# Performance work log

Hardware: AMD Instinct MI355X
Metric: run time of the kernel (lower is better)

## Reference

```python
import jax, jax.numpy as jnp
import numpy as np

ALPHA = 0.9      # synapse decay
BETA = 0.85      # membrane decay
THRESH = 1.0     # spike threshold
T = 100          # simulation_time
SCALE = 100.0    # SuperSpike surrogate scale

@jax.custom_vjp
def spike(x):
    # Heaviside step forward, fast-sigmoid surrogate gradient (Zenke & Ganguli 2018)
    return (x > 0).astype(x.dtype)

def _spike_fwd(x):
    return spike(x), x

def _spike_bwd(x, g):
    return (g / (SCALE * jnp.abs(x) + 1.0) ** 2,)

spike.defvjp(_spike_fwd, _spike_bwd)


def setup_inputs() -> dict:
    key = jax.random.key(0)
    k1, k2, k3, k4 = jax.random.split(key, 4)
    B = 1024
    shape = [784, 1024, 1024, 10]
    inp = {"input_data": jax.random.uniform(k1, (B, shape[0]), jnp.float32)}
    for i, (kk, (a, b)) in enumerate(zip([k2, k3, k4], zip(shape[:-1], shape[1:]))):
        # init: normal with std = weight_scale / sqrt(fan_in)
        inp[f"W{i}"] = jax.random.normal(kk, (a, b), jnp.float32) / np.sqrt(a)
    return inp


def reference(input_data, W0, W1, W2):
    Ws = [W0, W1, W2]
    B = input_data.shape[0]
    syn0 = [jnp.zeros((B, W.shape[1]), jnp.float32) for W in Ws]
    mem0 = [jnp.zeros((B, W.shape[1]), jnp.float32) for W in Ws]

    def step(carry, _):
        syn, mem = carry
        new_syn, new_mem = [], []
        x = input_data  # encoding='constant': same input every timestep
        for l, W in enumerate(Ws):
            h = x @ W  # [B, out_l]
            if l < len(Ws) - 1:
                # hidden LIF layers: threshold on OLD membrane, spike propagates
                # to the next layer within the same timestep
                mthr = mem[l] - THRESH
                out = spike(mthr)
                rst = jax.lax.stop_gradient(out)  # reset path carries no gradient
                x = out
            else:
                # last layer with decoding='potential': no spiking, no reset
                rst = jnp.zeros_like(mem[l])
            # note: new_mem uses the OLD syn (pre-update), as in the original
            new_syn.append(ALPHA * syn[l] + h)
            new_mem.append(BETA * mem[l] + syn[l] - rst)
        return (new_syn, new_mem), None

    (syn, mem), _ = jax.lax.scan(step, (syn0, mem0), None, length=T)
    # decoding='potential': final membrane potential of the output layer
    return mem[-1]
```

## Files before the change

kernel.cpp:

```cpp
#include <hip/hip_runtime.h>
#include <hip/hip_bf16.h>
#include <stdint.h>
#include <math.h>

typedef unsigned short u16;
typedef unsigned int u32;
typedef unsigned long long u64;
typedef __attribute__((ext_vector_type(8))) short short8;
typedef __attribute__((ext_vector_type(4))) float f32x4;

static constexpr int BDIM  = 1024;
static constexpr int D_IN  = 784;
static constexpr int D_H   = 1024;
static constexpr int D_OUT = 10;
static constexpr int TSTEPS = 100;
static constexpr int K0SEG = 800;
static constexpr int K0TOT = 2400;
static constexpr int NELEM = 1024 * 1024;

#define AL 0.9f
#define BE 0.85f

__device__ __forceinline__ void gld16(const void* g, void* l) {
  __builtin_amdgcn_global_load_lds(
      (const __attribute__((address_space(1))) u32*)g,
      (__attribute__((address_space(3))) u32*)l, 16, 0, 0);
}
__device__ __forceinline__ u16 f2bf(float v) {
  __hip_bfloat16 h = __float2bfloat16(v);
  u16 r; __builtin_memcpy(&r, &h, 2); return r;
}
__device__ __forceinline__ float bf2f(u16 b) {
  __hip_bfloat16 h; __builtin_memcpy(&h, &b, 2); return __bfloat162float(h);
}

__device__ __forceinline__ int stg_rot(int l) { return (((l & 3) - (l >> 3)) & 3) << 3; }
__device__ __forceinline__ int rd_rot(int l) {
  return (((l >> 4) + ((l & 15) >> 1)) & 3) << 3;
}

__global__ void prep0(const float* __restrict__ inp, const float* __restrict__ W0,
                      u16* __restrict__ A0, u16* __restrict__ BT0) {
  int kp = blockIdx.x * 256 + threadIdx.x;
  if (kp >= K0TOT) return;
  int row = blockIdx.y;
  int seg = kp / K0SEG;
  int kk  = kp - seg * K0SEG;
  float av = (kk < D_IN) ? inp[row * D_IN + kk] : 0.f;
  u16 ahi = f2bf(av);
  u16 alo = f2bf(av - bf2f(ahi));
  A0[(size_t)row * K0TOT + kp] = (seg < 2) ? ahi : alo;
  float wv = (kk < D_IN) ? W0[kk * D_H + row] : 0.f;
  u16 whi = f2bf(wv);
  u16 wlo = f2bf(wv - bf2f(whi));
  BT0[(size_t)row * K0TOT + kp] = (seg == 0) ? whi : ((seg == 1) ? wlo : whi);
}

__global__ void prep1(const float* __restrict__ W1, u16* __restrict__ W1h,
                      u16* __restrict__ W1l) {
  int k = blockIdx.x * 256 + threadIdx.x;
  int n = blockIdx.y;
  float v = W1[(size_t)k * D_H + n];
  u16 hi = f2bf(v);
  W1h[(size_t)n * D_H + k] = hi;
  W1l[(size_t)n * D_H + k] = f2bf(v - bf2f(hi));
}

template <int KTOT>
__global__ __launch_bounds__(256) void gemm_bt_t(
    const u16* __restrict__ A, const u16* __restrict__ BT, float* __restrict__ C) {
  constexpr int N = 1024, NBN = 8;
  __shared__ u16 As[128 * 32];
  __shared__ u16 Bs[128 * 32];
  const int nwg = gridDim.x;
  const int bid = blockIdx.x;
  const int wg = (bid & 7) * (nwg >> 3) + (bid >> 3);
  const int bm = wg / NBN, bn = wg - bm * NBN;
  const int tid = threadIdx.x;
  const int w = tid >> 6, l = tid & 63;
  const int wm = w & 1, wn = w >> 1;
  const int srow = l >> 2;
  const int scol = stg_rot(l);
  const size_t m0 = (size_t)bm * 128, n0 = (size_t)bn * 128;
  const int r0 = w * 32;

  const u16* aP0 = &A[(m0 + r0 + srow) * KTOT + scol];
  const u16* aP1 = &A[(m0 + r0 + 16 + srow) * KTOT + scol];
  const u16* bP0 = &BT[(n0 + r0 + srow) * KTOT + scol];
  const u16* bP1 = &BT[(n0 + r0 + 16 + srow) * KTOT + scol];

  const int ps = rd_rot(l);

  f32x4 acc[4][4] = {};

  for (int kt = 0; kt < KTOT; kt += 32) {
    __syncthreads();
    gld16(aP0 + kt, &As[(r0) * 32]);
    gld16(aP1 + kt, &As[(r0 + 16) * 32]);
    gld16(bP0 + kt, &Bs[(r0) * 32]);
    gld16(bP1 + kt, &Bs[(r0 + 16) * 32]);
    __syncthreads();

    short8 a[4], b[4];
#pragma unroll
    for (int m = 0; m < 4; m++)
      a[m] = *(const short8*)&As[(wm * 64 + m * 16 + (l & 15)) * 32 + ps];
#pragma unroll
    for (int n = 0; n < 4; n++)
      b[n] = *(const short8*)&Bs[(wn * 64 + n * 16 + (l & 15)) * 32 + ps];
#pragma unroll
    for (int m = 0; m < 4; m++)
#pragma unroll
      for (int n = 0; n < 4; n++)
        acc[m][n] = __builtin_amdgcn_mfma_f32_16x16x32_bf16(a[m], b[n], acc[m][n], 0, 0, 0);
  }

  const int rr = (l >> 4) * 4, cc = l & 15;
#pragma unroll
  for (int m = 0; m < 4; m++)
#pragma unroll
    for (int n = 0; n < 4; n++) {
      size_t row = m0 + wm * 64 + m * 16 + rr;
      size_t col = n0 + wn * 64 + n * 16 + cc;
#pragma unroll
      for (int j = 0; j < 4; j++)
        C[(row + j) * (size_t)N + col] = acc[m][n][j];
    }
}

__global__ __launch_bounds__(256) void gemm_dual2(
    const u16* __restrict__ A, const u16* __restrict__ Bh, const u16* __restrict__ Bl,
    float* __restrict__ C) {
  constexpr int N = 1024, K = 1024, NT = K / 32;
  __shared__ u16 lds[3 * 12288];
  const int nwg = gridDim.x;
  const int bid = blockIdx.x;
  const int wg = (bid & 7) * (nwg >> 3) + (bid >> 3);
  const int bm = wg >> 3, bn = wg & 7;
  const int tid = threadIdx.x;
  const int w = tid >> 6, l = tid & 63;
  const int wm = w >> 1, wn = w & 1;
  const size_t m0 = (size_t)bm * 128, n0 = (size_t)bn * 128;

  const int srow0 = (w * 2 + 0) * 16 + (l >> 2);
  const int srow1 = (w * 2 + 1) * 16 + (l >> 2);
  const int scol  = stg_rot(l);
  const u16* aS0 = A  + (m0 + srow0) * K + scol;
  const u16* aS1 = A  + (m0 + srow1) * K + scol;
  const u16* hS0 = Bh + (n0 + srow0) * K + scol;
  const u16* hS1 = Bh + (n0 + srow1) * K + scol;
  const u16* lS0 = Bl + (n0 + srow0) * K + scol;
  const u16* lS1 = Bl + (n0 + srow1) * K + scol;
  const int d0 = (w * 2 + 0) * 512;
  const int d1 = (w * 2 + 1) * 512;

  const int rrow = l & 15;
  const int ps = rd_rot(l);

  f32x4 acc[4][4] = {};

  auto STAGE = [&](int ts) {
    u16* Lb = &lds[(ts % 3) * 12288];
    const int ko = ts * 32;
    gld16(aS0 + ko, Lb + d0);
    gld16(aS1 + ko, Lb + d1);
    gld16(hS0 + ko, Lb + 4096 + d0);
    gld16(hS1 + ko, Lb + 4096 + d1);
    gld16(lS0 + ko, Lb + 8192 + d0);
    gld16(lS1 + ko, Lb + 8192 + d1);
  };

  STAGE(0);
  STAGE(1);
  asm volatile("s_waitcnt vmcnt(6)" ::: "memory");
  __builtin_amdgcn_sched_barrier(0);
  __builtin_amdgcn_s_barrier();

  for (int t = 0; t < NT; ++t) {
    const u16* Lb = &lds[(t % 3) * 12288];
    short8 a[4], bh[4], bl[4];
#pragma unroll
    for (int m = 0; m < 4; m++)
      a[m] = *(const short8*)&Lb[(wm * 64 + m * 16 + rrow) * 32 + ps];
#pragma unroll
    for (int n = 0; n < 4; n++) {
      bh[n] = *(const short8*)&Lb[4096 + (wn * 64 + n * 16 + rrow) * 32 + ps];
      bl[n] = *(const short8*)&Lb[8192 + (wn * 64 + n * 16 + rrow) * 32 + ps];
    }
    if (t + 2 < NT) {
      STAGE(t + 2);
      asm volatile("s_waitcnt vmcnt(6)" ::: "memory");
    } else {
      asm volatile("s_waitcnt vmcnt(0)" ::: "memory");
    }
    __builtin_amdgcn_sched_barrier(0);
    __builtin_amdgcn_s_barrier();
    __builtin_amdgcn_s_setprio(1);
#pragma unroll
    for (int m = 0; m < 4; m++)
#pragma unroll
      for (int n = 0; n < 4; n++)
        acc[m][n] = __builtin_amdgcn_mfma_f32_16x16x32_bf16(a[m], bh[n], acc[m][n], 0, 0, 0);
#pragma unroll
    for (int m = 0; m < 4; m++)
#pragma unroll
      for (int n = 0; n < 4; n++)
        acc[m][n] = __builtin_amdgcn_mfma_f32_16x16x32_bf16(a[m], bl[n], acc[m][n], 0, 0, 0);
    __builtin_amdgcn_s_setprio(0);
    __builtin_amdgcn_s_barrier();
  }

  const int rr = (l >> 4) * 4, cc = l & 15;
#pragma unroll
  for (int m = 0; m < 4; m++)
#pragma unroll
    for (int n = 0; n < 4; n++) {
      size_t row = m0 + wm * 64 + m * 16 + rr;
      size_t col = n0 + wn * 64 + n * 16 + cc;
#pragma unroll
      for (int j = 0; j < 4; j++)
        C[(row + j) * (size_t)N + col] = acc[m][n][j];
    }
}

__global__ void scan0(const float* __restrict__ Hconst,
                      float* __restrict__ syn_g, float* __restrict__ mem_g,
                      u64* __restrict__ S, int Tc) {
  int e4 = blockIdx.x * 256 + threadIdx.x;
  int e = e4 * 4;
  float4 syn = *(const float4*)&syn_g[e];
  float4 mem = *(const float4*)&mem_g[e];
  float4 hc = *(const float4*)&Hconst[e];
  for (int t = 0; t < Tc; t++) {
    bool s0 = mem.x > 1.0f, s1 = mem.y > 1.0f, s2 = mem.z > 1.0f, s3 = mem.w > 1.0f;
    u64 sp = (s0 ? 0x3F80ull : 0) | (s1 ? 0x3F800000ull : 0) |
             (s2 ? (0x3F80ull << 32) : 0) | (s3 ? (0x3F80ull << 48) : 0);
    S[(size_t)t * (NELEM / 4) + e4] = sp;
    float ns0 = AL * syn.x + hc.x, ns1 = AL * syn.y + hc.y;
    float ns2 = AL * syn.z + hc.z, ns3 = AL * syn.w + hc.w;
    float nm0 = BE * mem.x + syn.x - (s0 ? 1.0f : 0.0f);
    float nm1 = BE * mem.y + syn.y - (s1 ? 1.0f : 0.0f);
    float nm2 = BE * mem.z + syn.z - (s2 ? 1.0f : 0.0f);
    float nm3 = BE * mem.w + syn.w - (s3 ? 1.0f : 0.0f);
    syn.x = ns0; syn.y = ns1; syn.z = ns2; syn.w = ns3;
    mem.x = nm0; mem.y = nm1; mem.z = nm2; mem.w = nm3;
  }
  *(float4*)&syn_g[e] = syn;
  *(float4*)&mem_g[e] = mem;
}

__global__ void scan1z(const float* __restrict__ Hseq,
                       float* __restrict__ syn_g, float* __restrict__ mem_g,
                       float* __restrict__ z_g, int Tc, float cA0, float cB0) {
  int e4 = blockIdx.x * 256 + threadIdx.x;
  int e = e4 * 4;
  float4 syn = *(const float4*)&syn_g[e];
  float4 mem = *(const float4*)&mem_g[e];
  float4 z   = *(const float4*)&z_g[e];
  float cA = cA0, cB = cB0;
  for (int t = 0; t < Tc; t++) {
    float4 h = *(const float4*)&Hseq[(size_t)t * NELEM + e];
    float c = (cA - cB) * 20.0f;
    bool s0 = mem.x > 1.0f, s1 = mem.y > 1.0f, s2 = mem.z > 1.0f, s3 = mem.w > 1.0f;
    z.x += s0 ? c : 0.0f;
    z.y += s1 ? c : 0.0f;
    z.z += s2 ? c : 0.0f;
    z.w += s3 ? c : 0.0f;
    float ns0 = AL * syn.x + h.x, ns1 = AL * syn.y + h.y;
    float ns2 = AL * syn.z + h.z, ns3 = AL * syn.w + h.w;
    float nm0 = BE * mem.x + syn.x - (s0 ? 1.0f : 0.0f);
    float nm1 = BE * mem.y + syn.y - (s1 ? 1.0f : 0.0f);
    float nm2 = BE * mem.z + syn.z - (s2 ? 1.0f : 0.0f);
    float nm3 = BE * mem.w + syn.w - (s3 ? 1.0f : 0.0f);
    syn.x = ns0; syn.y = ns1; syn.z = ns2; syn.w = ns3;
    mem.x = nm0; mem.y = nm1; mem.z = nm2; mem.w = nm3;
    cA *= (1.0f / AL); cB *= (1.0f / BE);
  }
  *(float4*)&syn_g[e] = syn;
  *(float4*)&mem_g[e] = mem;
  *(float4*)&z_g[e] = z;
}

__global__ __launch_bounds__(256) void zgemm(const float* __restrict__ z,
                                             const float* __restrict__ W2,
                                             float* __restrict__ out) {
  __shared__ float red[256][10];
  const int b = blockIdx.x;
  const int t = threadIdx.x;
  float local[10];
#pragma unroll
  for (int j = 0; j < 10; j++) local[j] = 0.f;
  for (int k = t; k < D_H; k += 256) {
    float zv = z[(size_t)b * D_H + k];
    const float* wrow = &W2[(size_t)k * D_OUT];
#pragma unroll
    for (int j = 0; j < 10; j++) local[j] += zv * wrow[j];
  }
#pragma unroll
  for (int j = 0; j < 10; j++) red[t][j] = local[j];
  __syncthreads();
  for (int s = 128; s > 0; s >>= 1) {
    if (t < s)
#pragma unroll
      for (int j = 0; j < 10; j++) red[t][j] += red[t + s][j];
    __syncthreads();
  }
  if (t < 10) out[b * D_OUT + t] = red[0][t];
}

__global__ void diag(float* out, float v) {
  if (threadIdx.x == 0 && blockIdx.x == 0) out[0] = v;
}

extern "C" void kernel_launch(void* const* d_in, const int* in_sizes, int n_in,
                              void* d_out, int out_size, void* d_ws, size_t ws_size,
                              hipStream_t stream) {
  (void)in_sizes; (void)n_in; (void)out_size;
  const float* inp = (const float*)d_in[0];
  const float* W0  = (const float*)d_in[1];
  const float* W1  = (const float*)d_in[2];
  const float* W2  = (const float*)d_in[3];
  float* out = (float*)d_out;

  uint8_t* base = (uint8_t*)d_ws;
  size_t off = 0;
  auto alloc = [&](size_t bytes) -> void* {
    void* r = base + off;
    off += (bytes + 255) & ~(size_t)255;
    return r;
  };

  float* H0   = (float*)alloc((size_t)NELEM * 4);
  float* syn0 = (float*)alloc((size_t)NELEM * 4);
  float* mem0 = (float*)alloc((size_t)NELEM * 4);
  float* syn1 = (float*)alloc((size_t)NELEM * 4);
  float* mem1 = (float*)alloc((size_t)NELEM * 4);
  float* zbuf = (float*)alloc((size_t)NELEM * 4);
  u16* A0  = (u16*)alloc((size_t)BDIM * K0TOT * 2);
  u16* BT0 = (u16*)alloc((size_t)D_H * K0TOT * 2);
  u16* W1h = (u16*)alloc((size_t)D_H * D_H * 2);
  u16* W1l = (u16*)alloc((size_t)D_H * D_H * 2);
  size_t fixedEnd = off;

  int Tc = 0;
  const int cand[8] = {50, 25, 20, 10, 5, 4, 2, 1};
  for (int i = 0; i < 8; i++) {
    size_t per = (size_t)cand[i] * ((size_t)NELEM * 2 + (size_t)NELEM * 4);
    if (fixedEnd + per + 16 * 256 <= ws_size) { Tc = cand[i]; break; }
  }
  if (Tc == 0) {
    diag<<<1, 1, 0, stream>>>(out, (float)ws_size);
    return;
  }
  u16*   S0c = (u16*)alloc((size_t)Tc * NELEM * 2);
  float* H1c = (float*)alloc((size_t)Tc * NELEM * 4);

  hipMemsetAsync(syn0, 0, (size_t)5 * NELEM * 4, stream);

  prep0<<<dim3(10, BDIM), 256, 0, stream>>>(inp, W0, A0, BT0);
  prep1<<<dim3(4, D_H), 256, 0, stream>>>(W1, W1h, W1l);

  gemm_bt_t<K0TOT><<<dim3(8 * 8), 256, 0, stream>>>(A0, BT0, H0);

  const int nc = TSTEPS / Tc;
  for (int c = 0; c < nc; c++) {
    const int tbase = c * Tc;
    const float cA0 = (float)pow(0.9, (double)(TSTEPS - 1 - tbase));
    const float cB0 = (float)pow(0.85, (double)(TSTEPS - 1 - tbase));
    scan0<<<dim3(NELEM / 1024), 256, 0, stream>>>(H0, syn0, mem0, (u64*)S0c, Tc);
    gemm_dual2<<<dim3(Tc * 8 * 8), 256, 0, stream>>>(S0c, W1h, W1l, H1c);
    scan1z<<<dim3(NELEM / 1024), 256, 0, stream>>>(H1c, syn1, mem1, zbuf, Tc, cA0, cB0);
  }
  zgemm<<<dim3(BDIM), 256, 0, stream>>>(zbuf, W2, out);
}
```

Baseline: 617.1 us.

## Concatenate W1 hi/lo along K and use 256x128 tiles in hidden GEMM

The hi and lo bf16 halves of W1 are packed into a single K=2048 matrix. The A operand (spikes) is reused by wrapping k modulo 1024, so the split GEMM becomes one long-K GEMM. Each workgroup now computes a 256x128 tile with 8x4 accumulators, loading A and B in two half-stages per iteration, which cuts A reloads and LDS traffic per flop. The A0/BT0 buffers are aliased onto the S0c chunk buffer to save workspace, and Tc=1 is dropped as a candidate. The cost is more accumulator registers (launch bounds set to 2 waves) and fewer workgroups per chunk.

```diff
diff --git a/kernel.cpp b/kernel.cpp
--- a/kernel.cpp
+++ b/kernel.cpp
@@ -56,14 +56,12 @@
   BT0[(size_t)row * K0TOT + kp] = (seg == 0) ? whi : ((seg == 1) ? wlo : whi);
 }
 
-__global__ void prep1(const float* __restrict__ W1, u16* __restrict__ W1h,
-                      u16* __restrict__ W1l) {
+__global__ void prep1s(const float* __restrict__ W1, u16* __restrict__ W1s) {
   int k = blockIdx.x * 256 + threadIdx.x;
   int n = blockIdx.y;
-  float v = W1[(size_t)k * D_H + n];
+  float v = W1[(size_t)(k & 1023) * D_H + n];
   u16 hi = f2bf(v);
-  W1h[(size_t)n * D_H + k] = hi;
-  W1l[(size_t)n * D_H + k] = f2bf(v - bf2f(hi));
+  W1s[(size_t)n * 2048 + k] = (k < 1024) ? hi : f2bf(v - bf2f(hi));
 }
 
 template <int KTOT>
@@ -128,10 +126,9 @@
     }
 }
 
-__global__ __launch_bounds__(256) void gemm_dual2(
-    const u16* __restrict__ A, const u16* __restrict__ Bh, const u16* __restrict__ Bl,
-    float* __restrict__ C) {
-  constexpr int N = 1024, K = 1024, NT = K / 32;
+__global__ __launch_bounds__(256, 2) void gemm_dual5(
+    const u16* __restrict__ A, const u16* __restrict__ Bs2, float* __restrict__ C) {
+  constexpr int N = 1024, KA = 1024, KS = 2048, NT = 64;
   __shared__ u16 lds[3 * 12288];
   const int nwg = gridDim.x;
   const int bid = blockIdx.x;
@@ -140,55 +137,64 @@
   const int tid = threadIdx.x;
   const int w = tid >> 6, l = tid & 63;
   const int wm = w >> 1, wn = w & 1;
-  const size_t m0 = (size_t)bm * 128, n0 = (size_t)bn * 128;
-
-  const int srow0 = (w * 2 + 0) * 16 + (l >> 2);
-  const int srow1 = (w * 2 + 1) * 16 + (l >> 2);
-  const int scol  = stg_rot(l);
-  const u16* aS0 = A  + (m0 + srow0) * K + scol;
-  const u16* aS1 = A  + (m0 + srow1) * K + scol;
-  const u16* hS0 = Bh + (n0 + srow0) * K + scol;
-  const u16* hS1 = Bh + (n0 + srow1) * K + scol;
-  const u16* lS0 = Bl + (n0 + srow0) * K + scol;
-  const u16* lS1 = Bl + (n0 + srow1) * K + scol;
-  const int d0 = (w * 2 + 0) * 512;
-  const int d1 = (w * 2 + 1) * 512;
-
+  const size_t m0 = (size_t)bm * 256, n0 = (size_t)bn * 128;
+
+  const int srow = l >> 2;
+  const int scol = stg_rot(l);
+  const u16* aS = A   + (m0 + srow) * KA + scol;
+  const u16* bS = Bs2 + (n0 + srow) * KS + scol;
   const int rrow = l & 15;
   const int ps = rd_rot(l);
 
-  f32x4 acc[4][4] = {};
-
-  auto STAGE = [&](int ts) {
+  f32x4 acc[8][4] = {};
+
+  auto STAGE_A2 = [&](int ts, int half) {
     u16* Lb = &lds[(ts % 3) * 12288];
+    const int ko = (ts & 31) * 32;
+    const int u0 = w * 4 + half * 2;
+    gld16(aS + (size_t)u0 * 16 * KA + ko, Lb + u0 * 512);
+    gld16(aS + (size_t)(u0 + 1) * 16 * KA + ko, Lb + (u0 + 1) * 512);
+  };
+  auto STAGE_B1 = [&](int ts, int half) {
+    u16* Lb = &lds[(ts % 3) * 12288] + 8192;
     const int ko = ts * 32;
-    gld16(aS0 + ko, Lb + d0);
-    gld16(aS1 + ko, Lb + d1);
-    gld16(hS0 + ko, Lb + 4096 + d0);
-    gld16(hS1 + ko, Lb + 4096 + d1);
-    gld16(lS0 + ko, Lb + 8192 + d0);
-    gld16(lS1 + ko, Lb + 8192 + d1);
+    const int u = w * 2 + half;
+    gld16(bS + (size_t)u * 16 * KS + ko, Lb + u * 512);
   };
 
-  STAGE(0);
-  STAGE(1);
+  STAGE_A2(0, 0); STAGE_A2(0, 1); STAGE_B1(0, 0); STAGE_B1(0, 1);
+  STAGE_A2(1, 0); STAGE_A2(1, 1); STAGE_B1(1, 0); STAGE_B1(1, 1);
   asm volatile("s_waitcnt vmcnt(6)" ::: "memory");
   __builtin_amdgcn_sched_barrier(0);
   __builtin_amdgcn_s_barrier();
 
   for (int t = 0; t < NT; ++t) {
-    const u16* Lb = &lds[(t % 3) * 12288];
-    short8 a[4], bh[4], bl[4];
-#pragma unroll
-    for (int m = 0; m < 4; m++)
-      a[m] = *(const short8*)&Lb[(wm * 64 + m * 16 + rrow) * 32 + ps];
-#pragma unroll
-    for (int n = 0; n < 4; n++) {
-      bh[n] = *(const short8*)&Lb[4096 + (wn * 64 + n * 16 + rrow) * 32 + ps];
-      bl[n] = *(const short8*)&Lb[8192 + (wn * 64 + n * 16 + rrow) * 32 + ps];
-    }
+    const u16* LA = &lds[(t % 3) * 12288];
+    const u16* LB = LA + 8192;
+    short8 a[4], b[4];
+#pragma unroll
+    for (int m = 0; m < 4; m++)
+      a[m] = *(const short8*)&LA[(wm * 128 + m * 16 + rrow) * 32 + ps];
+#pragma unroll
+    for (int n = 0; n < 4; n++)
+      b[n] = *(const short8*)&LB[(wn * 64 + n * 16 + rrow) * 32 + ps];
+    if (t + 2 < NT) { STAGE_A2(t + 2, 0); STAGE_B1(t + 2, 0); }
+    __builtin_amdgcn_sched_barrier(0);
+    __builtin_amdgcn_s_barrier();
+    __builtin_amdgcn_s_setprio(1);
+#pragma unroll
+    for (int m = 0; m < 4; m++)
+#pragma unroll
+      for (int n = 0; n < 4; n++)
+        acc[m][n] = __builtin_amdgcn_mfma_f32_16x16x32_bf16(a[m], b[n], acc[m][n], 0, 0, 0);
+    __builtin_amdgcn_s_setprio(0);
+    __builtin_amdgcn_s_barrier();
+    short8 a2[4];
+#pragma unroll
+    for (int m = 0; m < 4; m++)
+      a2[m] = *(const short8*)&LA[(wm * 128 + (m + 4) * 16 + rrow) * 32 + ps];
     if (t + 2 < NT) {
-      STAGE(t + 2);
+      STAGE_A2(t + 2, 1); STAGE_B1(t + 2, 1);
       asm volatile("s_waitcnt vmcnt(6)" ::: "memory");
     } else {
       asm volatile("s_waitcnt vmcnt(0)" ::: "memory");
@@ -200,22 +206,17 @@
     for (int m = 0; m < 4; m++)
 #pragma unroll
       for (int n = 0; n < 4; n++)
-        acc[m][n] = __builtin_amdgcn_mfma_f32_16x16x32_bf16(a[m], bh[n], acc[m][n], 0, 0, 0);
-#pragma unroll
-    for (int m = 0; m < 4; m++)
-#pragma unroll
-      for (int n = 0; n < 4; n++)
-        acc[m][n] = __builtin_amdgcn_mfma_f32_16x16x32_bf16(a[m], bl[n], acc[m][n], 0, 0, 0);
+        acc[m + 4][n] = __builtin_amdgcn_mfma_f32_16x16x32_bf16(a2[m], b[n], acc[m + 4][n], 0, 0, 0);
     __builtin_amdgcn_s_setprio(0);
     __builtin_amdgcn_s_barrier();
   }
 
   const int rr = (l >> 4) * 4, cc = l & 15;
 #pragma unroll
-  for (int m = 0; m < 4; m++)
+  for (int m = 0; m < 8; m++)
 #pragma unroll
     for (int n = 0; n < 4; n++) {
-      size_t row = m0 + wm * 64 + m * 16 + rr;
+      size_t row = m0 + wm * 128 + m * 16 + rr;
       size_t col = n0 + wn * 64 + n * 16 + cc;
 #pragma unroll
       for (int j = 0; j < 4; j++)
@@ -336,15 +337,12 @@
   float* syn1 = (float*)alloc((size_t)NELEM * 4);
   float* mem1 = (float*)alloc((size_t)NELEM * 4);
   float* zbuf = (float*)alloc((size_t)NELEM * 4);
-  u16* A0  = (u16*)alloc((size_t)BDIM * K0TOT * 2);
-  u16* BT0 = (u16*)alloc((size_t)D_H * K0TOT * 2);
-  u16* W1h = (u16*)alloc((size_t)D_H * D_H * 2);
-  u16* W1l = (u16*)alloc((size_t)D_H * D_H * 2);
+  u16* W1s = (u16*)alloc((size_t)D_H * 2048 * 2);
   size_t fixedEnd = off;
 
   int Tc = 0;
-  const int cand[8] = {50, 25, 20, 10, 5, 4, 2, 1};
-  for (int i = 0; i < 8; i++) {
+  const int cand[7] = {50, 25, 20, 10, 5, 4, 2};
+  for (int i = 0; i < 7; i++) {
     size_t per = (size_t)cand[i] * ((size_t)NELEM * 2 + (size_t)NELEM * 4);
     if (fixedEnd + per + 16 * 256 <= ws_size) { Tc = cand[i]; break; }
   }
@@ -354,11 +352,13 @@
   }
   u16*   S0c = (u16*)alloc((size_t)Tc * NELEM * 2);
   float* H1c = (float*)alloc((size_t)Tc * NELEM * 4);
+  u16* A0  = (u16*)S0c;
+  u16* BT0 = A0 + (size_t)BDIM * K0TOT;
 
   hipMemsetAsync(syn0, 0, (size_t)5 * NELEM * 4, stream);
 
   prep0<<<dim3(10, BDIM), 256, 0, stream>>>(inp, W0, A0, BT0);
-  prep1<<<dim3(4, D_H), 256, 0, stream>>>(W1, W1h, W1l);
+  prep1s<<<dim3(8, D_H), 256, 0, stream>>>(W1, W1s);
 
   gemm_bt_t<K0TOT><<<dim3(8 * 8), 256, 0, stream>>>(A0, BT0, H0);
 
@@ -368,7 +368,7 @@
     const float cA0 = (float)pow(0.9, (double)(TSTEPS - 1 - tbase));
     const float cB0 = (float)pow(0.85, (double)(TSTEPS - 1 - tbase));
     scan0<<<dim3(NELEM / 1024), 256, 0, stream>>>(H0, syn0, mem0, (u64*)S0c, Tc);
-    gemm_dual2<<<dim3(Tc * 8 * 8), 256, 0, stream>>>(S0c, W1h, W1l, H1c);
+    gemm_dual5<<<dim3(Tc * 32), 256, 0, stream>>>(S0c, W1s, H1c);
     scan1z<<<dim3(NELEM / 1024), 256, 0, stream>>>(H1c, syn1, mem1, zbuf, Tc, cA0, cB0);
   }
   zgemm<<<dim3(BDIM), 256, 0, stream>>>(zbuf, W2, out);
```

Result: slower. 640.9 us (+3.9%).

## Fuse scan kernels across chunks, retile layer-0 GEMM to 64x64 with pipelining

Applied to the files above, without the earlier changes.

The layer-0 GEMM now uses 64x64 tiles across 256 workgroups instead of 64, and streams K through a 5-deep LDS ring filled by asynchronous global-to-LDS loads. This targets the poor CU occupancy of the old 64-block launch. The layer-1 scan for the current chunk and the layer-0 scan for the next chunk are merged into one launch, which cuts kernel launches and lets the two run concurrently. The layer-0 staging buffers now alias the chunk workspace, which frees memory for larger time chunks. That aliasing depends on prep0 and the first GEMM finishing before scan0k overwrites S0c, which holds because the stream is in-order.

```diff
diff --git a/kernel.cpp b/kernel.cpp
--- a/kernel.cpp
+++ b/kernel.cpp
@@ -67,61 +67,76 @@
 }
 
 template <int KTOT>
-__global__ __launch_bounds__(256) void gemm_bt_t(
+__global__ __launch_bounds__(256) void gemm_bt64(
     const u16* __restrict__ A, const u16* __restrict__ BT, float* __restrict__ C) {
-  constexpr int N = 1024, NBN = 8;
-  __shared__ u16 As[128 * 32];
-  __shared__ u16 Bs[128 * 32];
+  constexpr int N = 1024, NT = KTOT / 32;
+  constexpr int BUF = 4096;
+  __shared__ u16 lds[5 * BUF];
   const int nwg = gridDim.x;
   const int bid = blockIdx.x;
   const int wg = (bid & 7) * (nwg >> 3) + (bid >> 3);
-  const int bm = wg / NBN, bn = wg - bm * NBN;
+  const int bm = wg >> 4, bn = wg & 15;
   const int tid = threadIdx.x;
   const int w = tid >> 6, l = tid & 63;
-  const int wm = w & 1, wn = w >> 1;
+  const int wm = w >> 1, wn = w & 1;
+  const size_t m0 = (size_t)bm * 64, n0 = (size_t)bn * 64;
+
   const int srow = l >> 2;
   const int scol = stg_rot(l);
-  const size_t m0 = (size_t)bm * 128, n0 = (size_t)bn * 128;
-  const int r0 = w * 32;
-
-  const u16* aP0 = &A[(m0 + r0 + srow) * KTOT + scol];
-  const u16* aP1 = &A[(m0 + r0 + 16 + srow) * KTOT + scol];
-  const u16* bP0 = &BT[(n0 + r0 + srow) * KTOT + scol];
-  const u16* bP1 = &BT[(n0 + r0 + 16 + srow) * KTOT + scol];
-
+  const u16* aS = A  + (m0 + w * 16 + srow) * KTOT + scol;
+  const u16* bS = BT + (n0 + w * 16 + srow) * KTOT + scol;
+  const int dd = w * 512;
+
+  const int rrow = l & 15;
   const int ps = rd_rot(l);
 
-  f32x4 acc[4][4] = {};
-
-  for (int kt = 0; kt < KTOT; kt += 32) {
-    __syncthreads();
-    gld16(aP0 + kt, &As[(r0) * 32]);
-    gld16(aP1 + kt, &As[(r0 + 16) * 32]);
-    gld16(bP0 + kt, &Bs[(r0) * 32]);
-    gld16(bP1 + kt, &Bs[(r0 + 16) * 32]);
-    __syncthreads();
-
-    short8 a[4], b[4];
-#pragma unroll
-    for (int m = 0; m < 4; m++)
-      a[m] = *(const short8*)&As[(wm * 64 + m * 16 + (l & 15)) * 32 + ps];
-#pragma unroll
-    for (int n = 0; n < 4; n++)
-      b[n] = *(const short8*)&Bs[(wn * 64 + n * 16 + (l & 15)) * 32 + ps];
-#pragma unroll
-    for (int m = 0; m < 4; m++)
-#pragma unroll
-      for (int n = 0; n < 4; n++)
+  f32x4 acc[2][2] = {};
+
+  auto STAGE = [&](int ts) {
+    u16* Lb = &lds[(ts % 5) * BUF];
+    const int ko = ts * 32;
+    gld16(aS + ko, Lb + dd);
+    gld16(bS + ko, Lb + 2048 + dd);
+  };
+
+  STAGE(0); STAGE(1); STAGE(2); STAGE(3);
+  asm volatile("s_waitcnt vmcnt(6)" ::: "memory");
+  __builtin_amdgcn_sched_barrier(0);
+  __builtin_amdgcn_s_barrier();
+
+  for (int t = 0; t < NT; ++t) {
+    const u16* LA = &lds[(t % 5) * BUF];
+    const u16* LB = LA + 2048;
+    short8 a[2], b[2];
+#pragma unroll
+    for (int m = 0; m < 2; m++)
+      a[m] = *(const short8*)&LA[(wm * 32 + m * 16 + rrow) * 32 + ps];
+#pragma unroll
+    for (int n = 0; n < 2; n++)
+      b[n] = *(const short8*)&LB[(wn * 32 + n * 16 + rrow) * 32 + ps];
+    if (t + 4 < NT) {
+      STAGE(t + 4);
+      asm volatile("s_waitcnt vmcnt(6)" ::: "memory");
+    } else {
+      asm volatile("s_waitcnt vmcnt(0)" ::: "memory");
+    }
+    __builtin_amdgcn_sched_barrier(0);
+    __builtin_amdgcn_s_barrier();
+#pragma unroll
+    for (int m = 0; m < 2; m++)
+#pragma unroll
+      for (int n = 0; n < 2; n++)
         acc[m][n] = __builtin_amdgcn_mfma_f32_16x16x32_bf16(a[m], b[n], acc[m][n], 0, 0, 0);
+    __builtin_amdgcn_s_barrier();
   }
 
   const int rr = (l >> 4) * 4, cc = l & 15;
 #pragma unroll
-  for (int m = 0; m < 4; m++)
-#pragma unroll
-    for (int n = 0; n < 4; n++) {
-      size_t row = m0 + wm * 64 + m * 16 + rr;
-      size_t col = n0 + wn * 64 + n * 16 + cc;
+  for (int m = 0; m < 2; m++)
+#pragma unroll
+    for (int n = 0; n < 2; n++) {
+      size_t row = m0 + wm * 32 + m * 16 + rr;
+      size_t col = n0 + wn * 32 + n * 16 + cc;
 #pragma unroll
       for (int j = 0; j < 4; j++)
         C[(row + j) * (size_t)N + col] = acc[m][n][j];
@@ -223,10 +238,9 @@
     }
 }
 
-__global__ void scan0(const float* __restrict__ Hconst,
-                      float* __restrict__ syn_g, float* __restrict__ mem_g,
-                      u64* __restrict__ S, int Tc) {
-  int e4 = blockIdx.x * 256 + threadIdx.x;
+__device__ __forceinline__ void scan0_body(
+    int e4, const float* __restrict__ Hconst, float* __restrict__ syn_g,
+    float* __restrict__ mem_g, u64* __restrict__ S, int Tc) {
   int e = e4 * 4;
   float4 syn = *(const float4*)&syn_g[e];
   float4 mem = *(const float4*)&mem_g[e];
@@ -249,10 +263,10 @@
   *(float4*)&mem_g[e] = mem;
 }
 
-__global__ void scan1z(const float* __restrict__ Hseq,
-                       float* __restrict__ syn_g, float* __restrict__ mem_g,
-                       float* __restrict__ z_g, int Tc, float cA0, float cB0) {
-  int e4 = blockIdx.x * 256 + threadIdx.x;
+__device__ __forceinline__ void scan1z_body(
+    int e4, const float* __restrict__ Hseq, float* __restrict__ syn_g,
+    float* __restrict__ mem_g, float* __restrict__ z_g, int Tc,
+    float cA0, float cB0) {
   int e = e4 * 4;
   float4 syn = *(const float4*)&syn_g[e];
   float4 mem = *(const float4*)&mem_g[e];
@@ -281,6 +295,24 @@
   *(float4*)&z_g[e] = z;
 }
 
+__global__ void scan0k(const float* __restrict__ Hconst, float* __restrict__ syn_g,
+                       float* __restrict__ mem_g, u64* __restrict__ S, int Tc) {
+  scan0_body(blockIdx.x * 256 + threadIdx.x, Hconst, syn_g, mem_g, S, Tc);
+}
+
+__global__ void scanF(const float* __restrict__ H1c, float* __restrict__ syn1,
+                      float* __restrict__ mem1, float* __restrict__ z_g,
+                      int csC, float cA0, float cB0,
+                      const float* __restrict__ H0, float* __restrict__ syn0,
+                      float* __restrict__ mem0, u64* __restrict__ S0c, int csN) {
+  int b = blockIdx.x;
+  if (b < 1024) {
+    scan1z_body(b * 256 + threadIdx.x, H1c, syn1, mem1, z_g, csC, cA0, cB0);
+  } else {
+    scan0_body((b - 1024) * 256 + threadIdx.x, H0, syn0, mem0, S0c, csN);
+  }
+}
+
 __global__ __launch_bounds__(256) void zgemm(const float* __restrict__ z,
                                              const float* __restrict__ W2,
                                              float* __restrict__ out) {
@@ -336,15 +368,13 @@
   float* syn1 = (float*)alloc((size_t)NELEM * 4);
   float* mem1 = (float*)alloc((size_t)NELEM * 4);
   float* zbuf = (float*)alloc((size_t)NELEM * 4);
-  u16* A0  = (u16*)alloc((size_t)BDIM * K0TOT * 2);
-  u16* BT0 = (u16*)alloc((size_t)D_H * K0TOT * 2);
   u16* W1h = (u16*)alloc((size_t)D_H * D_H * 2);
   u16* W1l = (u16*)alloc((size_t)D_H * D_H * 2);
   size_t fixedEnd = off;
 
   int Tc = 0;
-  const int cand[8] = {50, 25, 20, 10, 5, 4, 2, 1};
-  for (int i = 0; i < 8; i++) {
+  const int cand[7] = {50, 34, 25, 20, 10, 5, 4};
+  for (int i = 0; i < 7; i++) {
     size_t per = (size_t)cand[i] * ((size_t)NELEM * 2 + (size_t)NELEM * 4);
     if (fixedEnd + per + 16 * 256 <= ws_size) { Tc = cand[i]; break; }
   }
@@ -354,22 +384,29 @@
   }
   u16*   S0c = (u16*)alloc((size_t)Tc * NELEM * 2);
   float* H1c = (float*)alloc((size_t)Tc * NELEM * 4);
+  u16* A0  = (u16*)S0c;
+  u16* BT0 = A0 + (size_t)BDIM * K0TOT;
 
   hipMemsetAsync(syn0, 0, (size_t)5 * NELEM * 4, stream);
 
   prep0<<<dim3(10, BDIM), 256, 0, stream>>>(inp, W0, A0, BT0);
   prep1<<<dim3(4, D_H), 256, 0, stream>>>(W1, W1h, W1l);
 
-  gemm_bt_t<K0TOT><<<dim3(8 * 8), 256, 0, stream>>>(A0, BT0, H0);
-
-  const int nc = TSTEPS / Tc;
-  for (int c = 0; c < nc; c++) {
-    const int tbase = c * Tc;
-    const float cA0 = (float)pow(0.9, (double)(TSTEPS - 1 - tbase));
-    const float cB0 = (float)pow(0.85, (double)(TSTEPS - 1 - tbase));
-    scan0<<<dim3(NELEM / 1024), 256, 0, stream>>>(H0, syn0, mem0, (u64*)S0c, Tc);
-    gemm_dual2<<<dim3(Tc * 8 * 8), 256, 0, stream>>>(S0c, W1h, W1l, H1c);
-    scan1z<<<dim3(NELEM / 1024), 256, 0, stream>>>(H1c, syn1, mem1, zbuf, Tc, cA0, cB0);
+  gemm_bt64<K0TOT><<<dim3(256), 256, 0, stream>>>(A0, BT0, H0);
+
+  int done = 0;
+  const int cs0 = (TSTEPS < Tc) ? TSTEPS : Tc;
+  scan0k<<<dim3(NELEM / 1024), 256, 0, stream>>>(H0, syn0, mem0, (u64*)S0c, cs0);
+  while (done < TSTEPS) {
+    int csC = TSTEPS - done < Tc ? TSTEPS - done : Tc;
+    int rem = TSTEPS - done - csC;
+    int csN = rem < Tc ? rem : Tc;
+    const float cA0 = (float)pow(0.9, (double)(TSTEPS - 1 - done));
+    const float cB0 = (float)pow(0.85, (double)(TSTEPS - 1 - done));
+    gemm_dual2<<<dim3(csC * 64), 256, 0, stream>>>(S0c, W1h, W1l, H1c);
+    scanF<<<dim3(csN > 0 ? 2048 : 1024), 256, 0, stream>>>(
+        H1c, syn1, mem1, zbuf, csC, cA0, cB0, H0, syn0, mem0, (u64*)S0c, csN);
+    done += csC;
   }
   zgemm<<<dim3(BDIM), 256, 0, stream>>>(zbuf, W2, out);
 }
```

Result: faster. 534.4 us (-13.4%).
